# Performance work log

Measured on AMD Instinct MI355X. Metric: run time of the kernel, lower is better.

The kernel has to match this reference:

```python
import jax, jax.numpy as jnp
import numpy as np

B, S, HIDDEN = 2, 2048, 2048
HEADS, GROUPS, KVC = 16, 4, 128
HPG = HEADS // GROUPS  # heads per group
LAYER_INDEX = 2
SOFTMAX_SCALE = KVC ** -0.5
ROPE_THETA = 10000.0


def _rope_tables(seq_len, dim, dtype=jnp.float32):
    inv_freq = 1.0 / (ROPE_THETA ** (jnp.arange(0, dim, 2, dtype=jnp.float32) / dim))
    t = jnp.arange(seq_len, dtype=jnp.float32)
    freqs = jnp.outer(t, inv_freq)  # [S, dim/2]
    return jnp.cos(freqs).astype(dtype), jnp.sin(freqs).astype(dtype)


def _apply_rope(x, cos, sin):
    # x: [b, s, h, d]; rotate-half (GPT-NeoX style)
    d2 = x.shape[-1] // 2
    x1, x2 = x[..., :d2], x[..., d2:]
    c = cos[None, :, None, :]
    s = sin[None, :, None, :]
    return jnp.concatenate([x1 * c - x2 * s, x2 * c + x1 * s], axis=-1)


def setup_inputs() -> dict:
    key = jax.random.key(0)
    k1, k2, k3, k4 = jax.random.split(key, 4)
    std = HIDDEN ** -0.5
    return {
        "x": jax.random.normal(k1, (B, S, HIDDEN), dtype=jnp.float32),
        "w_q": jax.random.normal(k2, (HIDDEN, HEADS * KVC), dtype=jnp.float32) * std,
        "w_kv": jax.random.normal(k3, (HIDDEN, 2 * GROUPS * KVC), dtype=jnp.float32) * std,
        "w_dense": jax.random.normal(k4, (HEADS * KVC, HIDDEN), dtype=jnp.float32) * std,
    }


def reference(x, w_q, w_kv, w_dense):
    b, s, _ = x.shape
    # QKV projections
    q = (x @ w_q).reshape(b, s, HEADS, KVC)                 # [b,s,H,d]
    kv = (x @ w_kv).reshape(b, s, 2, GROUPS, KVC)
    k, v = kv[:, :, 0], kv[:, :, 1]                          # [b,s,G,d]
    # Rotary embeddings on q and k
    cos, sin = _rope_tables(s, KVC, x.dtype)
    q = _apply_rope(q, cos, sin)
    k = _apply_rope(k, cos, sin)
    # GQA attention with per-layer scaling trick:
    # scores computed at scale/softmax of layer_index, cast fp32, rescaled back.
    qg = q.reshape(b, s, GROUPS, HPG, KVC)
    scores = jnp.einsum("bqghd,bkgd->bghqk", qg, k) * (SOFTMAX_SCALE / LAYER_INDEX)
    scores = scores.astype(jnp.float32) * LAYER_INDEX
    # causal mask
    causal = jnp.tril(jnp.ones((s, s), dtype=bool))
    mask_value = jnp.finfo(jnp.float32).min
    scores = jnp.where(causal[None, None, None, :, :], scores, mask_value)
    probs = jax.nn.softmax(scores, axis=-1).astype(x.dtype)  # dropout p=0 (eval)
    ctx = jnp.einsum("bghqk,bkgd->bqghd", probs, v).reshape(b, s, HEADS * KVC)
    return ctx @ w_dense
```

## Files before the change

kernel.cpp:

```cpp
#include <hip/hip_runtime.h>
#include <hip/hip_bf16.h>
#include <stdint.h>

typedef unsigned short u16;
typedef __bf16 bf16x8 __attribute__((ext_vector_type(8)));
typedef float f32x4 __attribute__((ext_vector_type(4)));

#define S_LEN 2048
#define BATCH 2
#define NHEADS 16
#define NGROUPS 4
#define DHEAD 128
#define QKV_W 3072

__device__ __forceinline__ float bf2f(u16 u) {
  union { uint32_t i; float f; } v; v.i = ((uint32_t)u) << 16; return v.f;
}
__device__ __forceinline__ u16 f2bf(float f) {
  union { float f; uint32_t i; } v; v.f = f;
  uint32_t r = v.i + 0x7FFF + ((v.i >> 16) & 1);
  return (u16)(r >> 16);
}
__device__ __forceinline__ void llds16(const void* g, void* l) {
  __builtin_amdgcn_global_load_lds(
      (const __attribute__((address_space(1))) uint32_t*)g,
      (__attribute__((address_space(3))) uint32_t*)l, 16, 0, 0);
}

__global__ void rope_tables_k(float* __restrict__ cosT, float* __restrict__ sinT) {
  int i = blockIdx.x * 256 + threadIdx.x;
  int s = i >> 6, j = i & 63;
  float inv = exp2f(-(float)j * 0.20762050593045983f);
  float ang = (float)s * inv;
  float sv, cv;
  sincosf(ang, &sv, &cv);
  cosT[i] = cv; sinT[i] = sv;
}

__global__ void cvt_f32_bf16(const float* __restrict__ in, u16* __restrict__ out) {
  long i = ((long)blockIdx.x * 256 + threadIdx.x) * 4;
  float4 v = *(const float4*)(in + i);
  ushort4 o;
  o.x = f2bf(v.x); o.y = f2bf(v.y); o.z = f2bf(v.z); o.w = f2bf(v.w);
  *(ushort4*)(out + i) = o;
}

__global__ void transpose_f32_bf16(const float* __restrict__ in, u16* __restrict__ out,
                                   int R, int C) {
  __shared__ u16 tile[32][33];
  int c0 = blockIdx.x * 32, r0 = blockIdx.y * 32;
  int tx = threadIdx.x, ty = threadIdx.y;
  for (int i = 0; i < 32; i += 8)
    tile[ty + i][tx] = f2bf(in[(long)(r0 + ty + i) * C + c0 + tx]);
  __syncthreads();
  for (int i = 0; i < 32; i += 8)
    out[(long)(c0 + ty + i) * R + r0 + tx] = tile[tx][ty + i];
}

#define GFENCE() asm volatile("" ::: "memory")
#define MIDBAR() do { GFENCE(); __builtin_amdgcn_s_barrier(); \
    asm volatile("s_waitcnt lgkmcnt(0)" ::: "memory"); } while (0)
#define ENDBAR() do { GFENCE(); __builtin_amdgcn_s_barrier(); GFENCE(); } while (0)

__device__ __forceinline__ bf16x8 frag_ld(const __bf16* h, int wrow, int kk, int quad) {
  int b = ((wrow & 15) << 6) | (quad << 4);
  b ^= ((wrow >> 3) & 1) << 5;
  int off = ((((wrow >> 4) << 1) | kk) << 10) | b;
  return *(const bf16x8*)((const char*)h + off);
}

__device__ __forceinline__ void stage_u64(const u16* __restrict__ g, int K,
                                          __bf16* ldsu, int wv, int lane) {
  int bsrc = (lane << 4) ^ (((lane >> 5) & 1) << 5);
  int r = bsrc >> 6, c = (bsrc & 63) >> 1;
  int cb = (wv & 1) << 5;
  llds16(g + (long)((wv >> 1) * 16 + r) * K + cb + c, ldsu + wv * 512 + lane * 8);
}
__device__ __forceinline__ void stage_half(const u16* __restrict__ g, int K,
                                           __bf16* lhalf, int wv, int lane) {
  stage_u64(g, K, lhalf, wv, lane);
  stage_u64(g + (long)64 * K, K, lhalf + 4096, wv, lane);
}

__global__ __launch_bounds__(512) void gemm_btw(
    const u16* __restrict__ A, const u16* __restrict__ Bt, u16* __restrict__ C,
    int M, int N, int K) {
  __shared__ __align__(16) __bf16 Abuf[2][16384];
  __shared__ __align__(16) __bf16 Bbuf[2][12288];
  const int tid = threadIdx.x;
  const int wv = tid >> 6, lane = tid & 63;
  const int quad = lane >> 4, l16 = lane & 15;
  const int wr = wv >> 2, wc = wv & 3;

  const int nwg = gridDim.x * gridDim.y;
  const int orig = blockIdx.y * gridDim.x + blockIdx.x;
  const int swz = (orig & 7) * (nwg >> 3) + (orig >> 3);
  const int bx = swz % gridDim.x, by = swz / gridDim.x;
  const int bm = by * 256, bn = bx * 192;

  const u16* Abase = A + (long)bm * K;
  const u16* Bbase = Bt + (long)bn * K;
  const int NT = K >> 6;

  f32x4 acc[8][3] = {};

#pragma unroll
  for (int t = 0; t < 2; ++t) {
#pragma unroll
    for (int u = 0; u < 4; ++u)
      stage_u64(Abase + (long)u * 64 * K + t * 64, K, &Abuf[t][u * 4096], wv, lane);
#pragma unroll
    for (int u = 0; u < 3; ++u)
      stage_u64(Bbase + (long)u * 64 * K + t * 64, K, &Bbuf[t][u * 4096], wv, lane);
  }
  asm volatile("s_waitcnt vmcnt(7)" ::: "memory");
  __builtin_amdgcn_s_barrier();
  GFENCE();

  for (int kt = 0; kt < NT; ++kt) {
    const int buf = kt & 1;
    const __bf16* Ah = &Abuf[buf][wr * 8192];
    const __bf16* Bh = &Bbuf[buf][0];
    const int bn0 = wc * 48;
    const bool pre = (kt + 2 < NT);
    bf16x8 aF[4][2], bF[3][2];

#pragma unroll
    for (int m = 0; m < 4; ++m) {
      aF[m][0] = frag_ld(Ah, m * 16 + l16, 0, quad);
      aF[m][1] = frag_ld(Ah, m * 16 + l16, 1, quad);
    }
    bF[0][0] = frag_ld(Bh, bn0 + l16, 0, quad);
    bF[0][1] = frag_ld(Bh, bn0 + l16, 1, quad);
    MIDBAR();
    __builtin_amdgcn_s_setprio(1);
#pragma unroll
    for (int m = 0; m < 4; ++m) {
      acc[m][0] = __builtin_amdgcn_mfma_f32_16x16x32_bf16(aF[m][0], bF[0][0], acc[m][0], 0, 0, 0);
      acc[m][0] = __builtin_amdgcn_mfma_f32_16x16x32_bf16(aF[m][1], bF[0][1], acc[m][0], 0, 0, 0);
    }
    __builtin_amdgcn_s_setprio(0);
    ENDBAR();

#pragma unroll
    for (int n = 1; n < 3; ++n) {
      bF[n][0] = frag_ld(Bh, bn0 + n * 16 + l16, 0, quad);
      bF[n][1] = frag_ld(Bh, bn0 + n * 16 + l16, 1, quad);
    }
    MIDBAR();
    __builtin_amdgcn_s_setprio(1);
#pragma unroll
    for (int m = 0; m < 4; ++m)
#pragma unroll
      for (int n = 1; n < 3; ++n) {
        acc[m][n] = __builtin_amdgcn_mfma_f32_16x16x32_bf16(aF[m][0], bF[n][0], acc[m][n], 0, 0, 0);
        acc[m][n] = __builtin_amdgcn_mfma_f32_16x16x32_bf16(aF[m][1], bF[n][1], acc[m][n], 0, 0, 0);
      }
    __builtin_amdgcn_s_setprio(0);
    ENDBAR();

#pragma unroll
    for (int m = 0; m < 4; ++m) {
      aF[m][0] = frag_ld(Ah, 64 + m * 16 + l16, 0, quad);
      aF[m][1] = frag_ld(Ah, 64 + m * 16 + l16, 1, quad);
    }
    if (pre) {
#pragma unroll
      for (int u = 0; u < 3; ++u)
        stage_u64(Bbase + (long)u * 64 * K + (long)(kt + 2) * 64, K,
                  &Bbuf[buf][u * 4096], wv, lane);
    }
    MIDBAR();
    __builtin_amdgcn_s_setprio(1);
#pragma unroll
    for (int m = 0; m < 4; ++m)
#pragma unroll
      for (int n = 1; n < 3; ++n) {
        acc[4 + m][n] = __builtin_amdgcn_mfma_f32_16x16x32_bf16(aF[m][0], bF[n][0], acc[4 + m][n], 0, 0, 0);
        acc[4 + m][n] = __builtin_amdgcn_mfma_f32_16x16x32_bf16(aF[m][1], bF[n][1], acc[4 + m][n], 0, 0, 0);
      }
    __builtin_amdgcn_s_setprio(0);
    ENDBAR();

    if (pre) {
#pragma unroll
      for (int u = 0; u < 4; ++u)
        stage_u64(Abase + (long)u * 64 * K + (long)(kt + 2) * 64, K,
                  &Abuf[buf][u * 4096], wv, lane);
    }
    MIDBAR();
    __builtin_amdgcn_s_setprio(1);
#pragma unroll
    for (int m = 0; m < 4; ++m) {
      acc[4 + m][0] = __builtin_amdgcn_mfma_f32_16x16x32_bf16(aF[m][0], bF[0][0], acc[4 + m][0], 0, 0, 0);
      acc[4 + m][0] = __builtin_amdgcn_mfma_f32_16x16x32_bf16(aF[m][1], bF[0][1], acc[4 + m][0], 0, 0, 0);
    }
    __builtin_amdgcn_s_setprio(0);
    if (pre) { asm volatile("s_waitcnt vmcnt(7)" ::: "memory"); }
    else     { asm volatile("s_waitcnt vmcnt(0)" ::: "memory"); }
    ENDBAR();
  }

  const long colbase = (long)bn + wc * 48 + l16;
#pragma unroll
  for (int mt = 0; mt < 8; ++mt)
#pragma unroll
    for (int nt = 0; nt < 3; ++nt)
#pragma unroll
      for (int rr = 0; rr < 4; ++rr) {
        long row = bm + wr * 128 + mt * 16 + quad * 4 + rr;
        C[row * N + colbase + nt * 16] = f2bf(acc[mt][nt][rr]);
      }
}

__global__ __launch_bounds__(512) void gemm_bt8n(
    const u16* __restrict__ A, const u16* __restrict__ Bt, float* __restrict__ C,
    int M, int N, int K) {
  __shared__ __align__(16) __bf16 Abuf[2][16384];
  __shared__ __align__(16) __bf16 Bbuf[2][8192];
  const int tid = threadIdx.x;
  const int wv = tid >> 6, lane = tid & 63;
  const int quad = lane >> 4, l16 = lane & 15;
  const int wr = wv >> 2, wc = wv & 3;

  const int nwg = gridDim.x * gridDim.y;
  const int orig = blockIdx.y * gridDim.x + blockIdx.x;
  const int swz = (orig & 7) * (nwg >> 3) + (orig >> 3);
  const int bx = swz % gridDim.x, by = swz / gridDim.x;
  const int bm = by * 256, bn = bx * 128;

  const u16* Abase = A + (long)bm * K;
  const u16* Bbase = Bt + (long)bn * K;
  const int NT = K >> 6;

  f32x4 acc[8][2] = {};

  stage_half(Abase, K, &Abuf[0][0], wv, lane);
  stage_half(Abase + (long)128 * K, K, &Abuf[0][8192], wv, lane);
  stage_half(Bbase, K, &Bbuf[0][0], wv, lane);
  stage_half(Abase + 64, K, &Abuf[1][0], wv, lane);
  stage_half(Abase + (long)128 * K + 64, K, &Abuf[1][8192], wv, lane);
  stage_half(Bbase + 64, K, &Bbuf[1][0], wv, lane);
  asm volatile("s_waitcnt vmcnt(0)" ::: "memory");
  __builtin_amdgcn_s_barrier();
  GFENCE();

  for (int kt = 0; kt < NT; ++kt) {
    const int buf = kt & 1;
    const __bf16* Ah = &Abuf[buf][wr * 8192];
    const __bf16* Bh = &Bbuf[buf][0];
    bf16x8 aF[4][2], bF[2][2];

#pragma unroll
    for (int m = 0; m < 4; ++m) {
      aF[m][0] = frag_ld(Ah, m * 16 + l16, 0, quad);
      aF[m][1] = frag_ld(Ah, m * 16 + l16, 1, quad);
    }
#pragma unroll
    for (int n = 0; n < 2; ++n) {
      bF[n][0] = frag_ld(Bh, wc * 32 + n * 16 + l16, 0, quad);
      bF[n][1] = frag_ld(Bh, wc * 32 + n * 16 + l16, 1, quad);
    }
    if (kt >= 1 && kt + 1 < NT) {
      const u16* p = Abase + (long)(kt + 1) * 64;
      stage_half(p, K, &Abuf[(kt + 1) & 1][0], wv, lane);
      stage_half(p + (long)128 * K, K, &Abuf[(kt + 1) & 1][8192], wv, lane);
    }
    MIDBAR();
    __builtin_amdgcn_s_setprio(1);
#pragma unroll
    for (int m = 0; m < 4; ++m)
#pragma unroll
      for (int n = 0; n < 2; ++n) {
        acc[m][n] = __builtin_amdgcn_mfma_f32_16x16x32_bf16(aF[m][0], bF[n][0], acc[m][n], 0, 0, 0);
        acc[m][n] = __builtin_amdgcn_mfma_f32_16x16x32_bf16(aF[m][1], bF[n][1], acc[m][n], 0, 0, 0);
      }
    __builtin_amdgcn_s_setprio(0);
    ENDBAR();

#pragma unroll
    for (int m = 0; m < 4; ++m) {
      aF[m][0] = frag_ld(Ah, 64 + m * 16 + l16, 0, quad);
      aF[m][1] = frag_ld(Ah, 64 + m * 16 + l16, 1, quad);
    }
    if (kt + 2 < NT) {
      stage_half(Bbase + (long)(kt + 2) * 64, K, &Bbuf[buf][0], wv, lane);
    }
    MIDBAR();
    __builtin_amdgcn_s_setprio(1);
#pragma unroll
    for (int m = 0; m < 4; ++m)
#pragma unroll
      for (int n = 0; n < 2; ++n) {
        acc[4 + m][n] = __builtin_amdgcn_mfma_f32_16x16x32_bf16(aF[m][0], bF[n][0], acc[4 + m][n], 0, 0, 0);
        acc[4 + m][n] = __builtin_amdgcn_mfma_f32_16x16x32_bf16(aF[m][1], bF[n][1], acc[4 + m][n], 0, 0, 0);
      }
    __builtin_amdgcn_s_setprio(0);
    if (kt + 2 < NT) { asm volatile("s_waitcnt vmcnt(2)" ::: "memory"); }
    else             { asm volatile("s_waitcnt vmcnt(0)" ::: "memory"); }
    ENDBAR();
  }

  const long colbase = (long)bn + wc * 32 + l16;
#pragma unroll
  for (int mt = 0; mt < 8; ++mt)
#pragma unroll
    for (int nt = 0; nt < 2; ++nt)
#pragma unroll
      for (int rr = 0; rr < 4; ++rr) {
        long row = bm + wr * 128 + mt * 16 + quad * 4 + rr;
        C[row * N + colbase + nt * 16] = acc[mt][nt][rr];
      }
}

__global__ void rope_k_k(const u16* __restrict__ qkv, u16* __restrict__ Kb,
                         const float* __restrict__ cosT, const float* __restrict__ sinT) {
  long i = (long)blockIdx.x * 256 + threadIdx.x;
  int j = i & 63;
  long rest = i >> 6;
  int g = rest & 3;
  long bs = rest >> 2;
  int s = bs & (S_LEN - 1);
  int b = (int)(bs >> 11);
  long src = bs * QKV_W + 2048 + g * 128 + j;
  float x1 = bf2f(qkv[src]), x2 = bf2f(qkv[src + 64]);
  float c = cosT[s * 64 + j], sn = sinT[s * 64 + j];
  long dst = ((long)(b * NGROUPS + g) * S_LEN + s) * DHEAD + j;
  Kb[dst] = f2bf(x1 * c - x2 * sn);
  Kb[dst + 64] = f2bf(x2 * c + x1 * sn);
}

__global__ void v_trans_k(const u16* __restrict__ qkv, u16* __restrict__ Vt) {
  __shared__ u16 tile[32][33];
  int s0 = blockIdx.x * 32, d0 = blockIdx.y * 32;
  int bg = blockIdx.z;
  int b = bg >> 2, g = bg & 3;
  int tx = threadIdx.x, ty = threadIdx.y;
  for (int i = 0; i < 32; i += 8) {
    long s = s0 + ty + i;
    tile[ty + i][tx] = qkv[((long)b * S_LEN + s) * QKV_W + 2560 + g * 128 + d0 + tx];
  }
  __syncthreads();
  for (int i = 0; i < 32; i += 8) {
    int d = d0 + ty + i;
    Vt[((long)(b * NGROUPS + g) * DHEAD + d) * S_LEN + s0 + tx] = tile[tx][ty + i];
  }
}

__global__ __launch_bounds__(512, 2) void attn_k11(
    const u16* __restrict__ Q,
    const u16* __restrict__ Kb,
    const u16* __restrict__ Vt,
    const float* __restrict__ cosT, const float* __restrict__ sinT,
    u16* __restrict__ ctx) {
  __shared__ __align__(16) char smem[82432];
  __bf16* Ks   = (__bf16*)smem;
  __bf16* Vts  = (__bf16*)(smem + 32768);
  __bf16* Ps   = (__bf16*)(smem + 65536);
  float*  Psum = (float*)(smem + 81920);
  float*  scr  = (float*)smem;

  const int h = blockIdx.y, b = blockIdx.z, g = h >> 2;
  const int tx = blockIdx.x;
  const int tid = threadIdx.x, wv = tid >> 6, lane = tid & 63;
  const int quad = lane >> 4, l16 = lane & 15;
  const int rg = wv & 3;
  const int kh = wv >> 2;
  const float SCALE = 0.08838834764831845f;

  const long kbase = (long)(b * NGROUPS + g) * S_LEN * DHEAD;
  const long vbase = (long)(b * NGROUPS + g) * DHEAD * S_LEN;

  const int krow_off = lane >> 4;
  const int vrow_off = lane >> 3;

  const __bf16 oneb = (__bf16)((l16 == 0) ? 1.0f : 0.0f);
  const bf16x8 bones = {oneb, oneb, oneb, oneb, oneb, oneb, oneb, oneb};

  __bf16* Prg = Ps + rg * 2048;

  for (int pass = 0; pass < 2; ++pass) {
    const int tile = pass ? (15 - tx) : tx;
    const int q0 = tile * 128;
    const int nch = 2 * (tile + 1);

    bf16x8 aq[2][4];
#pragma unroll
    for (int m = 0; m < 2; ++m) {
      const int srow = q0 + rg * 32 + m * 16 + l16;
      const u16* qp = Q + (long)(b * S_LEN + srow) * QKV_W + h * DHEAD + quad * 8;
      bf16x8 raw[4];
#pragma unroll
      for (int ds = 0; ds < 4; ++ds)
        raw[ds] = *(const bf16x8*)(qp + ds * 32);
      const float* cb = cosT + srow * 64 + quad * 8;
      const float* sb = sinT + srow * 64 + quad * 8;
#pragma unroll
      for (int ds = 0; ds < 2; ++ds)
#pragma unroll
        for (int e = 0; e < 8; ++e) {
          float c = cb[ds * 32 + e], s = sb[ds * 32 + e];
          float lo = (float)raw[ds][e], hi = (float)raw[ds + 2][e];
          aq[m][ds][e]     = (__bf16)(lo * c - hi * s);
          aq[m][ds + 2][e] = (__bf16)(hi * c + lo * s);
        }
    }

#pragma unroll
    for (int i = 0; i < 2; ++i) {
      int r0 = wv * 8 + i * 4;
      int row = r0 + krow_off;
      int c = l16 ^ (row & 15);
      llds16(Kb + kbase + (long)row * DHEAD + c * 8, &Ks[r0 * 128 + lane * 8]);
    }
#pragma unroll
    for (int i = 0; i < 2; ++i) {
      int d0 = wv * 16 + i * 8;
      int row = d0 + vrow_off;
      int c = (lane & 7) ^ (row & 7);
      llds16(Vt + vbase + (long)row * S_LEN + c * 8, &Vts[d0 * 64 + lane * 8]);
    }
    __syncthreads();

    f32x4 Oacc[2][8] = {};
    f32x4 Osum[2] = {};
    const int rmin = q0 + rg * 32;

    for (int kc = 0; kc < nch; ++kc) {
      const int cur = kc & 1;
      if (kc + 1 < nch) {
        const int nxt = cur ^ 1;
#pragma unroll
        for (int i = 0; i < 2; ++i) {
          int r0 = wv * 8 + i * 4;
          int row = r0 + krow_off;
          int c = l16 ^ (row & 15);
          llds16(Kb + kbase + (long)((kc + 1) * 64 + row) * DHEAD + c * 8,
                 &Ks[nxt * 8192 + r0 * 128 + lane * 8]);
        }
#pragma unroll
        for (int i = 0; i < 2; ++i) {
          int d0 = wv * 16 + i * 8;
          int row = d0 + vrow_off;
          int c = (lane & 7) ^ (row & 7);
          llds16(Vt + vbase + (long)row * S_LEN + (kc + 1) * 64 + c * 8,
                 &Vts[nxt * 8192 + d0 * 64 + lane * 8]);
        }
      }

      const int kb0 = kc * 64 + kh * 32;
      const bool skip = kb0 > (rmin + 31);
      if (!skip) {
        f32x4 sacc[2][2] = {};
        __builtin_amdgcn_s_setprio(1);
#pragma unroll
        for (int ds = 0; ds < 4; ++ds) {
          int pos0 = ((ds * 4 + quad) ^ l16) * 8;
#pragma unroll
          for (int nt = 0; nt < 2; ++nt) {
            bf16x8 bk = *(const bf16x8*)&Ks[cur * 8192 + (kh * 32 + nt * 16 + l16) * 128 + pos0];
            sacc[0][nt] = __builtin_amdgcn_mfma_f32_16x16x32_bf16(aq[0][ds], bk, sacc[0][nt], 0, 0, 0);
            sacc[1][nt] = __builtin_amdgcn_mfma_f32_16x16x32_bf16(aq[1][ds], bk, sacc[1][nt], 0, 0, 0);
          }
        }
        __builtin_amdgcn_s_setprio(0);

        const bool need_mask = (kb0 + 31) > rmin;
        if (need_mask) {
#pragma unroll
          for (int m = 0; m < 2; ++m)
#pragma unroll
            for (int nt = 0; nt < 2; ++nt)
#pragma unroll
              for (int r = 0; r < 4; ++r) {
                int qrow = rmin + m * 16 + quad * 4 + r;
                int key = kb0 + nt * 16 + l16;
                float p = (key <= qrow) ? __expf(sacc[m][nt][r] * SCALE) : 0.f;
                int row = m * 16 + quad * 4 + r;
                int gq = kh * 4 + nt * 2 + (l16 >> 3);
                int pos = gq ^ (row & 7);
                Prg[row * 64 + pos * 8 + (l16 & 7)] = (__bf16)p;
              }
        } else {
#pragma unroll
          for (int m = 0; m < 2; ++m)
#pragma unroll
            for (int nt = 0; nt < 2; ++nt)
#pragma unroll
              for (int r = 0; r < 4; ++r) {
                float p = __expf(sacc[m][nt][r] * SCALE);
                int row = m * 16 + quad * 4 + r;
                int gq = kh * 4 + nt * 2 + (l16 >> 3);
                int pos = gq ^ (row & 7);
                Prg[row * 64 + pos * 8 + (l16 & 7)] = (__bf16)p;
              }
        }

        bf16x8 ap[2];
#pragma unroll
        for (int m = 0; m < 2; ++m) {
          int pos = (kh * 4 + quad) ^ (l16 & 7);
          ap[m] = *(const bf16x8*)&Prg[(m * 16 + l16) * 64 + pos * 8];
        }
        __builtin_amdgcn_s_setprio(1);
#pragma unroll
        for (int nt = 0; nt < 8; ++nt) {
          int pos = (((kh << 2) | quad) ^ (l16 & 7)) * 8;
          bf16x8 bv = *(const bf16x8*)&Vts[cur * 8192 + (nt * 16 + l16) * 64 + pos];
          Oacc[0][nt] = __builtin_amdgcn_mfma_f32_16x16x32_bf16(ap[0], bv, Oacc[0][nt], 0, 0, 0);
          Oacc[1][nt] = __builtin_amdgcn_mfma_f32_16x16x32_bf16(ap[1], bv, Oacc[1][nt], 0, 0, 0);
        }
#pragma unroll
        for (int m = 0; m < 2; ++m)
          Osum[m] = __builtin_amdgcn_mfma_f32_16x16x32_bf16(ap[m], bones, Osum[m], 0, 0, 0);
        __builtin_amdgcn_s_setprio(0);
      }

      __syncthreads();
    }

    if (kh == 1) {
      float* s = scr + rg * 4096;
#pragma unroll
      for (int m = 0; m < 2; ++m)
#pragma unroll
        for (int nt = 0; nt < 8; ++nt)
#pragma unroll
          for (int r = 0; r < 4; ++r)
            s[(m * 16 + quad * 4 + r) * 128 + nt * 16 + l16] = Oacc[m][nt][r];
      if (l16 == 0) {
#pragma unroll
        for (int m = 0; m < 2; ++m)
#pragma unroll
          for (int r = 0; r < 4; ++r)
            Psum[rg * 32 + m * 16 + quad * 4 + r] = Osum[m][r];
      }
    }
    __syncthreads();
    if (kh == 0) {
      float* s = scr + rg * 4096;
#pragma unroll
      for (int m = 0; m < 2; ++m) {
        float lsum[4];
#pragma unroll
        for (int r = 0; r < 4; ++r)
          lsum[r] = __shfl(Osum[m][r], quad << 4, 64) +
                    Psum[rg * 32 + m * 16 + quad * 4 + r];
        const long obase = ((long)(b * S_LEN + q0 + rg * 32 + m * 16) * NHEADS + h) * DHEAD;
#pragma unroll
        for (int nt = 0; nt < 8; ++nt)
#pragma unroll
          for (int r = 0; r < 4; ++r) {
            int lrow = quad * 4 + r;
            float v = Oacc[m][nt][r] + s[(m * 16 + lrow) * 128 + nt * 16 + l16];
            ctx[obase + (long)lrow * NHEADS * DHEAD + nt * 16 + l16] = f2bf(v / lsum[r]);
          }
      }
    }
    __syncthreads();
  }
}

extern "C" void kernel_launch(void* const* d_in, const int* in_sizes, int n_in,
                              void* d_out, int out_size, void* d_ws, size_t ws_size,
                              hipStream_t stream) {
  const float* x   = (const float*)d_in[0];
  const float* wq  = (const float*)d_in[1];
  const float* wkv = (const float*)d_in[2];
  const float* wd  = (const float*)d_in[3];
  float* out = (float*)d_out;

  char* ws = (char*)d_ws;
  float* cosT  = (float*)(ws + 0);
  float* sinT  = (float*)(ws + 524288);
  u16* wqkvT = (u16*)(ws + 1048576);
  u16* wdT   = (u16*)(ws + 13631488);
  u16* xb    = (u16*)(ws + 22020096);
  u16* qkv   = (u16*)(ws + 38797312);
  u16* Kb    = (u16*)(ws + 63963136);
  u16* Vt    = (u16*)(ws + 68157440);
  u16* ctx   = (u16*)(ws + 72351744);

  rope_tables_k<<<512, 256, 0, stream>>>(cosT, sinT);
  cvt_f32_bf16<<<8192, 256, 0, stream>>>(x, xb);
  transpose_f32_bf16<<<dim3(64, 64), dim3(32, 8), 0, stream>>>(wq, wqkvT, 2048, 2048);
  transpose_f32_bf16<<<dim3(32, 64), dim3(32, 8), 0, stream>>>(wkv, wqkvT + (long)2048 * 2048, 2048, 1024);
  transpose_f32_bf16<<<dim3(64, 64), dim3(32, 8), 0, stream>>>(wd, wdT, 2048, 2048);

  gemm_btw<<<dim3(16, 16), 512, 0, stream>>>(xb, wqkvT, qkv, 4096, 3072, 2048);

  rope_k_k<<<4096, 256, 0, stream>>>(qkv, Kb, cosT, sinT);
  v_trans_k<<<dim3(64, 4, 8), dim3(32, 8), 0, stream>>>(qkv, Vt);

  attn_k11<<<dim3(8, 16, 2), 512, 0, stream>>>(qkv, Kb, Vt, cosT, sinT, ctx);

  gemm_bt8n<<<dim3(16, 16), 512, 0, stream>>>(ctx, wdT, out, 4096, 2048, 2048);
}
```

Baseline: 284.9 us.

## Triple-buffer K/V tiles in attention with prefetch distance two

The attention kernel moves from double to triple buffering of the K and V^T LDS tiles and issues loads two chunks ahead. Instead of a full __syncthreads per chunk, each wave waits with s_waitcnt vmcnt on only the older load group and then hits a bare barrier. This aims to hide more global-to-LDS latency behind the MFMA work. It also pads the fp32 reduction scratch rows from 128 to 132 floats to cut LDS bank conflicts, and raises the LDS footprint to about 115 KB per block.

```diff
diff --git a/kernel.cpp b/kernel.cpp
--- a/kernel.cpp
+++ b/kernel.cpp
@@ -347,17 +347,17 @@
   }
 }
 
-__global__ __launch_bounds__(512, 2) void attn_k11(
+__global__ __launch_bounds__(512, 2) void attn_k12(
     const u16* __restrict__ Q,
     const u16* __restrict__ Kb,
     const u16* __restrict__ Vt,
     const float* __restrict__ cosT, const float* __restrict__ sinT,
     u16* __restrict__ ctx) {
-  __shared__ __align__(16) char smem[82432];
+  __shared__ __align__(16) char smem[115200];
   __bf16* Ks   = (__bf16*)smem;
-  __bf16* Vts  = (__bf16*)(smem + 32768);
-  __bf16* Ps   = (__bf16*)(smem + 65536);
-  float*  Psum = (float*)(smem + 81920);
+  __bf16* Vts  = (__bf16*)(smem + 49152);
+  __bf16* Ps   = (__bf16*)(smem + 98304);
+  float*  Psum = (float*)(smem + 114688);
   float*  scr  = (float*)smem;
 
   const int h = blockIdx.y, b = blockIdx.z, g = h >> 2;
@@ -406,46 +406,40 @@
         }
     }
 
-#pragma unroll
-    for (int i = 0; i < 2; ++i) {
-      int r0 = wv * 8 + i * 4;
-      int row = r0 + krow_off;
-      int c = l16 ^ (row & 15);
-      llds16(Kb + kbase + (long)row * DHEAD + c * 8, &Ks[r0 * 128 + lane * 8]);
-    }
-#pragma unroll
-    for (int i = 0; i < 2; ++i) {
-      int d0 = wv * 16 + i * 8;
-      int row = d0 + vrow_off;
-      int c = (lane & 7) ^ (row & 7);
-      llds16(Vt + vbase + (long)row * S_LEN + c * 8, &Vts[d0 * 64 + lane * 8]);
-    }
-    __syncthreads();
+#define STAGE_KV(c, bi) do {                                              \
+    _Pragma("unroll")                                                     \
+    for (int i = 0; i < 2; ++i) {                                         \
+      int r0 = wv * 8 + i * 4;                                            \
+      int row = r0 + krow_off;                                            \
+      int cc = l16 ^ (row & 15);                                          \
+      llds16(Kb + kbase + (long)((c) * 64 + row) * DHEAD + cc * 8,        \
+             &Ks[(bi) * 8192 + r0 * 128 + lane * 8]);                     \
+    }                                                                     \
+    _Pragma("unroll")                                                     \
+    for (int i = 0; i < 2; ++i) {                                         \
+      int d0 = wv * 16 + i * 8;                                           \
+      int row = d0 + vrow_off;                                            \
+      int cc = (lane & 7) ^ (row & 7);                                    \
+      llds16(Vt + vbase + (long)row * S_LEN + (c) * 64 + cc * 8,          \
+             &Vts[(bi) * 8192 + d0 * 64 + lane * 8]);                     \
+    }                                                                     \
+  } while (0)
+
+    STAGE_KV(0, 0);
+    STAGE_KV(1, 1);
+    asm volatile("s_waitcnt vmcnt(4)" ::: "memory");
+    GFENCE(); __builtin_amdgcn_s_barrier(); GFENCE();
 
     f32x4 Oacc[2][8] = {};
     f32x4 Osum[2] = {};
     const int rmin = q0 + rg * 32;
 
+    int cur = 0;
     for (int kc = 0; kc < nch; ++kc) {
-      const int cur = kc & 1;
-      if (kc + 1 < nch) {
-        const int nxt = cur ^ 1;
-#pragma unroll
-        for (int i = 0; i < 2; ++i) {
-          int r0 = wv * 8 + i * 4;
-          int row = r0 + krow_off;
-          int c = l16 ^ (row & 15);
-          llds16(Kb + kbase + (long)((kc + 1) * 64 + row) * DHEAD + c * 8,
-                 &Ks[nxt * 8192 + r0 * 128 + lane * 8]);
-        }
-#pragma unroll
-        for (int i = 0; i < 2; ++i) {
-          int d0 = wv * 16 + i * 8;
-          int row = d0 + vrow_off;
-          int c = (lane & 7) ^ (row & 7);
-          llds16(Vt + vbase + (long)row * S_LEN + (kc + 1) * 64 + c * 8,
-                 &Vts[nxt * 8192 + d0 * 64 + lane * 8]);
-        }
+      const bool pre = (kc + 2 < nch);
+      if (pre) {
+        int nb = cur + 2; if (nb >= 3) nb -= 3;
+        STAGE_KV(kc + 2, nb);
       }
 
       const int kb0 = kc * 64 + kh * 32;
@@ -516,18 +510,23 @@
         __builtin_amdgcn_s_setprio(0);
       }
 
-      __syncthreads();
-    }
+      if (pre) { asm volatile("s_waitcnt vmcnt(4)" ::: "memory"); }
+      else     { asm volatile("s_waitcnt vmcnt(0)" ::: "memory"); }
+      GFENCE(); __builtin_amdgcn_s_barrier(); GFENCE();
+
+      ++cur; if (cur >= 3) cur = 0;
+    }
+#undef STAGE_KV
 
     if (kh == 1) {
-      float* s = scr + rg * 4096;
+      float* s = scr + rg * 4224;
 #pragma unroll
       for (int m = 0; m < 2; ++m)
 #pragma unroll
         for (int nt = 0; nt < 8; ++nt)
 #pragma unroll
           for (int r = 0; r < 4; ++r)
-            s[(m * 16 + quad * 4 + r) * 128 + nt * 16 + l16] = Oacc[m][nt][r];
+            s[(m * 16 + quad * 4 + r) * 132 + nt * 16 + l16] = Oacc[m][nt][r];
       if (l16 == 0) {
 #pragma unroll
         for (int m = 0; m < 2; ++m)
@@ -538,7 +537,7 @@
     }
     __syncthreads();
     if (kh == 0) {
-      float* s = scr + rg * 4096;
+      float* s = scr + rg * 4224;
 #pragma unroll
       for (int m = 0; m < 2; ++m) {
         float lsum[4];
@@ -552,7 +551,7 @@
 #pragma unroll
           for (int r = 0; r < 4; ++r) {
             int lrow = quad * 4 + r;
-            float v = Oacc[m][nt][r] + s[(m * 16 + lrow) * 128 + nt * 16 + l16];
+            float v = Oacc[m][nt][r] + s[(m * 16 + lrow) * 132 + nt * 16 + l16];
             ctx[obase + (long)lrow * NHEADS * DHEAD + nt * 16 + l16] = f2bf(v / lsum[r]);
           }
       }
@@ -592,7 +591,7 @@
   rope_k_k<<<4096, 256, 0, stream>>>(qkv, Kb, cosT, sinT);
   v_trans_k<<<dim3(64, 4, 8), dim3(32, 8), 0, stream>>>(qkv, Vt);
 
-  attn_k11<<<dim3(8, 16, 2), 512, 0, stream>>>(qkv, Kb, Vt, cosT, sinT, ctx);
+  attn_k12<<<dim3(8, 16, 2), 512, 0, stream>>>(qkv, Kb, Vt, cosT, sinT, ctx);
 
   gemm_bt8n<<<dim3(16, 16), 512, 0, stream>>>(ctx, wdT, out, 4096, 2048, 2048);
 }
```

Result: no change. 286.0 us (+0.4%).

## Split dense GEMM k-step into four MFMA phases and pad attention reduction scratch

Applied to the files above, without the earlier changes.

The output-projection GEMM main loop is reorganized into four barrier-separated phases, each loading only one B fragment pair and issuing a quarter of the MFMAs. The A prefetch for tile kt+2 moves into the final phase, and the vmcnt waits are relaxed so more loads stay in flight across iterations. Separately, the attention kernel's cross-wave partial-output scratch uses a row stride of 132 floats instead of 128 to reduce LDS bank conflicts. The extra barriers add synchronization cost, and the changed wait counts have to match the number of outstanding loads exactly.

```diff
diff --git a/kernel.cpp b/kernel.cpp
--- a/kernel.cpp
+++ b/kernel.cpp
@@ -213,7 +213,7 @@
       }
 }
 
-__global__ __launch_bounds__(512) void gemm_bt8n(
+__global__ __launch_bounds__(512) void gemm_bt4n(
     const u16* __restrict__ A, const u16* __restrict__ Bt, float* __restrict__ C,
     int M, int N, int K) {
   __shared__ __align__(16) __bf16 Abuf[2][16384];
@@ -235,13 +235,13 @@
 
   f32x4 acc[8][2] = {};
 
-  stage_half(Abase, K, &Abuf[0][0], wv, lane);
-  stage_half(Abase + (long)128 * K, K, &Abuf[0][8192], wv, lane);
-  stage_half(Bbase, K, &Bbuf[0][0], wv, lane);
-  stage_half(Abase + 64, K, &Abuf[1][0], wv, lane);
-  stage_half(Abase + (long)128 * K + 64, K, &Abuf[1][8192], wv, lane);
-  stage_half(Bbase + 64, K, &Bbuf[1][0], wv, lane);
-  asm volatile("s_waitcnt vmcnt(0)" ::: "memory");
+#pragma unroll
+  for (int t = 0; t < 2; ++t) {
+    stage_half(Abase + t * 64, K, &Abuf[t][0], wv, lane);
+    stage_half(Abase + (long)128 * K + t * 64, K, &Abuf[t][8192], wv, lane);
+    stage_half(Bbase + t * 64, K, &Bbuf[t][0], wv, lane);
+  }
+  asm volatile("s_waitcnt vmcnt(6)" ::: "memory");
   __builtin_amdgcn_s_barrier();
   GFENCE();
 
@@ -249,6 +249,8 @@
     const int buf = kt & 1;
     const __bf16* Ah = &Abuf[buf][wr * 8192];
     const __bf16* Bh = &Bbuf[buf][0];
+    const int bn0 = wc * 32;
+    const bool pre = (kt + 2 < NT);
     bf16x8 aF[4][2], bF[2][2];
 
 #pragma unroll
@@ -256,25 +258,27 @@
       aF[m][0] = frag_ld(Ah, m * 16 + l16, 0, quad);
       aF[m][1] = frag_ld(Ah, m * 16 + l16, 1, quad);
     }
-#pragma unroll
-    for (int n = 0; n < 2; ++n) {
-      bF[n][0] = frag_ld(Bh, wc * 32 + n * 16 + l16, 0, quad);
-      bF[n][1] = frag_ld(Bh, wc * 32 + n * 16 + l16, 1, quad);
-    }
-    if (kt >= 1 && kt + 1 < NT) {
-      const u16* p = Abase + (long)(kt + 1) * 64;
-      stage_half(p, K, &Abuf[(kt + 1) & 1][0], wv, lane);
-      stage_half(p + (long)128 * K, K, &Abuf[(kt + 1) & 1][8192], wv, lane);
-    }
-    MIDBAR();
-    __builtin_amdgcn_s_setprio(1);
-#pragma unroll
-    for (int m = 0; m < 4; ++m)
-#pragma unroll
-      for (int n = 0; n < 2; ++n) {
-        acc[m][n] = __builtin_amdgcn_mfma_f32_16x16x32_bf16(aF[m][0], bF[n][0], acc[m][n], 0, 0, 0);
-        acc[m][n] = __builtin_amdgcn_mfma_f32_16x16x32_bf16(aF[m][1], bF[n][1], acc[m][n], 0, 0, 0);
-      }
+    bF[0][0] = frag_ld(Bh, bn0 + l16, 0, quad);
+    bF[0][1] = frag_ld(Bh, bn0 + l16, 1, quad);
+    MIDBAR();
+    __builtin_amdgcn_s_setprio(1);
+#pragma unroll
+    for (int m = 0; m < 4; ++m) {
+      acc[m][0] = __builtin_amdgcn_mfma_f32_16x16x32_bf16(aF[m][0], bF[0][0], acc[m][0], 0, 0, 0);
+      acc[m][0] = __builtin_amdgcn_mfma_f32_16x16x32_bf16(aF[m][1], bF[0][1], acc[m][0], 0, 0, 0);
+    }
+    __builtin_amdgcn_s_setprio(0);
+    ENDBAR();
+
+    bF[1][0] = frag_ld(Bh, bn0 + 16 + l16, 0, quad);
+    bF[1][1] = frag_ld(Bh, bn0 + 16 + l16, 1, quad);
+    MIDBAR();
+    __builtin_amdgcn_s_setprio(1);
+#pragma unroll
+    for (int m = 0; m < 4; ++m) {
+      acc[m][1] = __builtin_amdgcn_mfma_f32_16x16x32_bf16(aF[m][0], bF[1][0], acc[m][1], 0, 0, 0);
+      acc[m][1] = __builtin_amdgcn_mfma_f32_16x16x32_bf16(aF[m][1], bF[1][1], acc[m][1], 0, 0, 0);
+    }
     __builtin_amdgcn_s_setprio(0);
     ENDBAR();
 
@@ -283,21 +287,34 @@
       aF[m][0] = frag_ld(Ah, 64 + m * 16 + l16, 0, quad);
       aF[m][1] = frag_ld(Ah, 64 + m * 16 + l16, 1, quad);
     }
-    if (kt + 2 < NT) {
+    if (pre) {
       stage_half(Bbase + (long)(kt + 2) * 64, K, &Bbuf[buf][0], wv, lane);
     }
     MIDBAR();
     __builtin_amdgcn_s_setprio(1);
 #pragma unroll
-    for (int m = 0; m < 4; ++m)
-#pragma unroll
-      for (int n = 0; n < 2; ++n) {
-        acc[4 + m][n] = __builtin_amdgcn_mfma_f32_16x16x32_bf16(aF[m][0], bF[n][0], acc[4 + m][n], 0, 0, 0);
-        acc[4 + m][n] = __builtin_amdgcn_mfma_f32_16x16x32_bf16(aF[m][1], bF[n][1], acc[4 + m][n], 0, 0, 0);
-      }
-    __builtin_amdgcn_s_setprio(0);
-    if (kt + 2 < NT) { asm volatile("s_waitcnt vmcnt(2)" ::: "memory"); }
-    else             { asm volatile("s_waitcnt vmcnt(0)" ::: "memory"); }
+    for (int m = 0; m < 4; ++m) {
+      acc[4 + m][1] = __builtin_amdgcn_mfma_f32_16x16x32_bf16(aF[m][0], bF[1][0], acc[4 + m][1], 0, 0, 0);
+      acc[4 + m][1] = __builtin_amdgcn_mfma_f32_16x16x32_bf16(aF[m][1], bF[1][1], acc[4 + m][1], 0, 0, 0);
+    }
+    __builtin_amdgcn_s_setprio(0);
+    ENDBAR();
+
+    if (pre) {
+      const u16* p = Abase + (long)(kt + 2) * 64;
+      stage_half(p, K, &Abuf[buf][0], wv, lane);
+      stage_half(p + (long)128 * K, K, &Abuf[buf][8192], wv, lane);
+    }
+    MIDBAR();
+    __builtin_amdgcn_s_setprio(1);
+#pragma unroll
+    for (int m = 0; m < 4; ++m) {
+      acc[4 + m][0] = __builtin_amdgcn_mfma_f32_16x16x32_bf16(aF[m][0], bF[0][0], acc[4 + m][0], 0, 0, 0);
+      acc[4 + m][0] = __builtin_amdgcn_mfma_f32_16x16x32_bf16(aF[m][1], bF[0][1], acc[4 + m][0], 0, 0, 0);
+    }
+    __builtin_amdgcn_s_setprio(0);
+    if (pre) { asm volatile("s_waitcnt vmcnt(6)" ::: "memory"); }
+    else     { asm volatile("s_waitcnt vmcnt(0)" ::: "memory"); }
     ENDBAR();
   }
 
@@ -347,7 +364,7 @@
   }
 }
 
-__global__ __launch_bounds__(512, 2) void attn_k11(
+__global__ __launch_bounds__(512, 2) void attn_k13(
     const u16* __restrict__ Q,
     const u16* __restrict__ Kb,
     const u16* __restrict__ Vt,
@@ -520,14 +537,14 @@
     }
 
     if (kh == 1) {
-      float* s = scr + rg * 4096;
+      float* s = scr + rg * 4224;
 #pragma unroll
       for (int m = 0; m < 2; ++m)
 #pragma unroll
         for (int nt = 0; nt < 8; ++nt)
 #pragma unroll
           for (int r = 0; r < 4; ++r)
-            s[(m * 16 + quad * 4 + r) * 128 + nt * 16 + l16] = Oacc[m][nt][r];
+            s[(m * 16 + quad * 4 + r) * 132 + nt * 16 + l16] = Oacc[m][nt][r];
       if (l16 == 0) {
 #pragma unroll
         for (int m = 0; m < 2; ++m)
@@ -538,7 +555,7 @@
     }
     __syncthreads();
     if (kh == 0) {
-      float* s = scr + rg * 4096;
+      float* s = scr + rg * 4224;
 #pragma unroll
       for (int m = 0; m < 2; ++m) {
         float lsum[4];
@@ -552,7 +569,7 @@
 #pragma unroll
           for (int r = 0; r < 4; ++r) {
             int lrow = quad * 4 + r;
-            float v = Oacc[m][nt][r] + s[(m * 16 + lrow) * 128 + nt * 16 + l16];
+            float v = Oacc[m][nt][r] + s[(m * 16 + lrow) * 132 + nt * 16 + l16];
             ctx[obase + (long)lrow * NHEADS * DHEAD + nt * 16 + l16] = f2bf(v / lsum[r]);
           }
       }
@@ -592,7 +609,7 @@
   rope_k_k<<<4096, 256, 0, stream>>>(qkv, Kb, cosT, sinT);
   v_trans_k<<<dim3(64, 4, 8), dim3(32, 8), 0, stream>>>(qkv, Vt);
 
-  attn_k11<<<dim3(8, 16, 2), 512, 0, stream>>>(qkv, Kb, Vt, cosT, sinT, ctx);
-
-  gemm_bt8n<<<dim3(16, 16), 512, 0, stream>>>(ctx, wdT, out, 4096, 2048, 2048);
-}
+  attn_k13<<<dim3(8, 16, 2), 512, 0, stream>>>(qkv, Kb, Vt, cosT, sinT, ctx);
+
+  gemm_bt4n<<<dim3(16, 16), 512, 0, stream>>>(ctx, wdT, out, 4096, 2048, 2048);
+}
```

Result: no change. 290.6 us (+2.0%).
